# Optimization experiments

Measured on AMD Instinct MI355X. Metric: run time of the kernel, lower is better.

The kernel has to match this reference:

```python
import jax, jax.numpy as jnp
import numpy as np
import math

NH = 12      # num attention heads
WIN = 128    # one-sided sliding window
NG = 32      # number of global (prefix) tokens
NEG = -1e9
LN_EPS = 1e-12


def _layernorm(x, g, b):
    mu = jnp.mean(x, axis=-1, keepdims=True)
    var = jnp.mean(jnp.square(x - mu), axis=-1, keepdims=True)
    return (x - mu) * jax.lax.rsqrt(var + LN_EPS) * g + b


def _longformer_self_attn(h, am, Wq, bq, Wk, bk, Wv, bv):
    B, S, D = h.shape
    Dh = D // NH
    w = WIN
    C = S // w  # number of chunks

    def proj(Wm, bm):
        return (h @ Wm + bm).reshape(B, S, NH, Dh).transpose(0, 2, 1, 3)

    q = proj(Wq, bq) * (1.0 / math.sqrt(Dh))  # [B,H,S,Dh]
    k = proj(Wk, bk)
    v = proj(Wv, bv)

    # ---- banded (sliding window) scores, chunked: each query chunk sees 3w keys ----
    kp = jnp.pad(k, ((0, 0), (0, 0), (w, w), (0, 0)))
    vp = jnp.pad(v, ((0, 0), (0, 0), (w, w), (0, 0)))
    idx = jnp.arange(C)[:, None] * w + jnp.arange(3 * w)[None, :]  # [C,3w]
    k3 = kp[:, :, idx]  # [B,H,C,3w,Dh]
    v3 = vp[:, :, idx]
    qc = q.reshape(B, NH, C, w, Dh)
    band = jnp.einsum('bhcqd,bhckd->bhcqk', qc, k3)  # [B,H,C,w,3w]

    qpos = (jnp.arange(C) * w)[:, None, None] + jnp.arange(w)[None, :, None]  # [C,w,1]
    kpos = (idx - w)[:, None, :]  # [C,1,3w] absolute key positions
    valid = (jnp.abs(kpos - qpos) <= w) & (kpos >= NG) & (kpos < S)  # band, exclude global keys

    amp = jnp.pad(am, ((0, 0), (w, w)))
    am3 = amp[:, idx]  # [B,C,3w] additive mask gathered per chunk
    band = band + am3[:, None, :, None, :]
    band = jnp.where(valid[None, None], band, NEG)
    band = band.reshape(B, NH, S, 3 * w)

    # ---- every token also attends to the NG global tokens ----
    gsc = jnp.einsum('bhsd,bhgd->bhsg', q, k[:, :, :NG]) + am[:, None, None, :NG]

    logits = jnp.concatenate([band, gsc], axis=-1)  # [B,H,S,3w+NG]
    probs = jax.nn.softmax(logits, axis=-1)
    pb = probs[..., :3 * w].reshape(B, NH, C, w, 3 * w)
    out = jnp.einsum('bhcqk,bhckd->bhcqd', pb, v3).reshape(B, NH, S, Dh)
    out = out + jnp.einsum('bhsg,bhgd->bhsd', probs[..., 3 * w:], v[:, :, :NG])

    # ---- global tokens attend to everything ----
    gl = jnp.einsum('bhgd,bhsd->bhgs', q[:, :, :NG], k) + am[:, None, None, :]
    outg = jnp.einsum('bhgs,bhsd->bhgd', jax.nn.softmax(gl, axis=-1), v)

    ctx = jnp.concatenate([outg, out[:, :, NG:]], axis=2)  # [B,H,S,Dh]
    return ctx.transpose(0, 2, 1, 3).reshape(B, S, D)


def setup_inputs() -> dict:
    key = jax.random.key(0)
    ks = jax.random.split(key, 8)
    B, S, D, F = 2, 4096, 768, 3072
    p = lambda k_, sh: jax.random.normal(k_, sh, jnp.float32) * 0.02
    return {
        'hidden_states': jax.random.normal(ks[0], (B, S, D), jnp.float32),
        'attention_mask': jnp.zeros((B, S), jnp.float32),
        'Wq': p(ks[1], (D, D)), 'bq': jnp.zeros((D,), jnp.float32),
        'Wk': p(ks[2], (D, D)), 'bk': jnp.zeros((D,), jnp.float32),
        'Wv': p(ks[3], (D, D)), 'bv': jnp.zeros((D,), jnp.float32),
        'Wo': p(ks[4], (D, D)), 'bo': jnp.zeros((D,), jnp.float32),
        'ln1_g': jnp.ones((D,), jnp.float32), 'ln1_b': jnp.zeros((D,), jnp.float32),
        'Wi': p(ks[5], (D, F)), 'bi': jnp.zeros((F,), jnp.float32),
        'Wo2': p(ks[6], (F, D)), 'bo2': jnp.zeros((D,), jnp.float32),
        'ln2_g': jnp.ones((D,), jnp.float32), 'ln2_b': jnp.zeros((D,), jnp.float32),
    }


def reference(hidden_states, attention_mask, Wq, bq, Wk, bk, Wv, bv, Wo, bo,
              ln1_g, ln1_b, Wi, bi, Wo2, bo2, ln2_g, ln2_b):
    ctx = _longformer_self_attn(hidden_states, attention_mask, Wq, bq, Wk, bk, Wv, bv)
    attn_out = _layernorm(ctx @ Wo + bo + hidden_states, ln1_g, ln1_b)
    inter = jax.nn.gelu(attn_out @ Wi + bi, approximate=False)
    layer_out = _layernorm(inter @ Wo2 + bo2 + attn_out, ln2_g, ln2_b)
    return layer_out
```

## Files before the change

kernel.cpp:

```cpp
#include <hip/hip_runtime.h>
#include <math.h>

#define NHEAD 12
#define DH 64
#define S_LEN 4096
#define B_SZ 2
#define D_MODEL 768
#define FF_DIM 3072
#define WINSZ 128
#define NGLB 32
#define NEGV -1e9f
#define NQC 6291456L

typedef __attribute__((ext_vector_type(8))) short bf16x8;
typedef __attribute__((ext_vector_type(4))) float floatx4;

__device__ __forceinline__ unsigned short f2bf(float x) {
    union { float f; unsigned u; } v; v.f = x;
    unsigned r = v.u + 0x7fffu + ((v.u >> 16) & 1u);
    return (unsigned short)(r >> 16);
}
__device__ __forceinline__ float bf2f(unsigned short x) {
    union { unsigned u; float f; } v; v.u = ((unsigned)x) << 16;
    return v.f;
}

__device__ __forceinline__ void async_copy16(const unsigned short* g, unsigned short* l) {
    __builtin_amdgcn_global_load_lds(
        (const __attribute__((address_space(1))) void*)g,
        (__attribute__((address_space(3))) void*)l, 16, 0, 0);
}

__global__ __launch_bounds__(256) void prep_k(
    const float* __restrict__ Wq, const float* __restrict__ Wk,
    const float* __restrict__ Wv, const float* __restrict__ Wo,
    const float* __restrict__ Wi, const float* __restrict__ Wo2,
    unsigned short* __restrict__ wqt, unsigned short* __restrict__ wkt,
    unsigned short* __restrict__ wvt, unsigned short* __restrict__ wot,
    unsigned short* __restrict__ wit, unsigned short* __restrict__ wo2t,
    const float* __restrict__ bq, const float* __restrict__ bk,
    const float* __restrict__ bv, float* __restrict__ bcat,
    const float* __restrict__ hid, unsigned short* __restrict__ hidb)
{
    __shared__ float tile[32][33];
    const int bid = blockIdx.x;
    const int tx = threadIdx.x, ty = threadIdx.y;

    if (bid < 6912) {
        const float* src; unsigned short* dst; int K, N, nx, local; float scale = 1.f;
        if (bid < 576)       { src = Wq;  dst = wqt;  K = 768;  N = 768;  nx = 24; local = bid;        scale = 0.125f; }
        else if (bid < 1152) { src = Wk;  dst = wkt;  K = 768;  N = 768;  nx = 24; local = bid - 576;  }
        else if (bid < 1728) { src = Wv;  dst = wvt;  K = 768;  N = 768;  nx = 24; local = bid - 1152; }
        else if (bid < 2304) { src = Wo;  dst = wot;  K = 768;  N = 768;  nx = 24; local = bid - 1728; }
        else if (bid < 4608) { src = Wi;  dst = wit;  K = 768;  N = 3072; nx = 96; local = bid - 2304; }
        else                 { src = Wo2; dst = wo2t; K = 3072; N = 768;  nx = 24; local = bid - 4608; }
        const int n0 = (local % nx) * 32, k0 = (local / nx) * 32;
#pragma unroll
        for (int i = 0; i < 4; ++i)
            tile[ty + 8 * i][tx] = src[(long)(k0 + ty + 8 * i) * N + n0 + tx];
        __syncthreads();
#pragma unroll
        for (int i = 0; i < 4; ++i)
            dst[(long)(n0 + ty + 8 * i) * K + k0 + tx] = f2bf(tile[tx][ty + 8 * i] * scale);
    } else if (bid < 6921) {
        const int t = ty * 32 + tx;
        const int i = (bid - 6912) * 256 + t;
        if (i < 768) bcat[i] = bq[i] * 0.125f;
        else if (i < 1536) bcat[i] = bk[i - 768];
        else if (i < 2304) bcat[i] = bv[i - 1536];
    } else {
        const int t = ty * 32 + tx;
        const long i = ((long)(bid - 6921) * 256 + t) * 4;
        float4 v = *(const float4*)(hid + i);
        ushort4 o;
        o.x = f2bf(v.x); o.y = f2bf(v.y); o.z = f2bf(v.z); o.w = f2bf(v.w);
        *(ushort4*)(hidb + i) = o;
    }
}

__global__ __launch_bounds__(256) void vt_k(
    const unsigned short* __restrict__ v, unsigned short* __restrict__ vt)
{
    const int bh = blockIdx.y;
    const int s0 = blockIdx.x * 32;
    const int w = threadIdx.x >> 6, lane = threadIdx.x & 63;
    const unsigned short* src = v + ((long)bh * S_LEN + s0 + w * 8) * DH + lane;
    unsigned short r[8];
#pragma unroll
    for (int j = 0; j < 8; ++j) r[j] = src[j * DH];
    unsigned short* dst = vt + ((long)bh * DH + lane) * S_LEN + s0 + w * 8;
    ushort4 lo, hi;
    lo.x = r[0]; lo.y = r[1]; lo.z = r[2]; lo.w = r[3];
    hi.x = r[4]; hi.y = r[5]; hi.z = r[6]; hi.w = r[7];
    *(ushort4*)dst = lo;
    *(ushort4*)(dst + 4) = hi;
}

template <int EPI>
__global__ __launch_bounds__(256) void gemm_bf(
    const unsigned short* __restrict__ A, const unsigned short* __restrict__ BT,
    const float* __restrict__ bias, void* __restrict__ out,
    int M, int N, int K, int nx)
{
    __shared__ unsigned short As[2][128 * 32];
    __shared__ unsigned short Bs[2][128 * 32];
    const int tid = threadIdx.x;
    const int wave = tid >> 6, lane = tid & 63;
    const int t8 = (blockIdx.x & 7) * (gridDim.x >> 3) + (blockIdx.x >> 3);
    const int m0 = (t8 / nx) * 128, n0 = (t8 % nx) * 128;
    const int wr = (wave >> 1) * 64, wc = (wave & 1) * 64;

    floatx4 acc[4][4];
#pragma unroll
    for (int i = 0; i < 4; ++i)
#pragma unroll
        for (int j = 0; j < 4; ++j) acc[i][j] = (floatx4){0.f, 0.f, 0.f, 0.f};

    const int srow = lane >> 2;
    const int schk = (((lane & 3) ^ (srow & 3))) * 8;
    const int r = lane & 15;
    const int q8 = ((lane >> 4) ^ (lane & 3)) * 8;

    const int NT = K >> 5;
    const unsigned short* aSrc0 = A  + (long)(m0 + wave * 32 + srow) * K + schk;
    const unsigned short* aSrc1 = A  + (long)(m0 + wave * 32 + 16 + srow) * K + schk;
    const unsigned short* bSrc0 = BT + (long)(n0 + wave * 32 + srow) * K + schk;
    const unsigned short* bSrc1 = BT + (long)(n0 + wave * 32 + 16 + srow) * K + schk;
    const int g0 = wave * 1024, g1 = wave * 1024 + 512;

    async_copy16(aSrc0, &As[0][g0]);
    async_copy16(bSrc0, &Bs[0][g0]);
    async_copy16(aSrc1, &As[0][g1]);
    async_copy16(bSrc1, &Bs[0][g1]);
    __syncthreads();

    for (int t = 0; t < NT; ++t) {
        const int cur = t & 1;
        if (t + 1 < NT) {
            const int k0 = (t + 1) << 5;
            async_copy16(aSrc0 + k0, &As[cur ^ 1][g0]);
            async_copy16(bSrc0 + k0, &Bs[cur ^ 1][g0]);
            async_copy16(aSrc1 + k0, &As[cur ^ 1][g1]);
            async_copy16(bSrc1 + k0, &Bs[cur ^ 1][g1]);
        }
        __builtin_amdgcn_sched_barrier(0);

        bf16x8 af[4], bfr[4];
#pragma unroll
        for (int i = 0; i < 4; ++i) {
            af[i]  = *(const bf16x8*)&As[cur][(wr + i * 16 + r) * 32 + q8];
            bfr[i] = *(const bf16x8*)&Bs[cur][(wc + i * 16 + r) * 32 + q8];
        }
        __builtin_amdgcn_s_setprio(1);
#pragma unroll
        for (int i = 0; i < 4; ++i)
#pragma unroll
            for (int j = 0; j < 4; ++j)
                acc[i][j] = __builtin_amdgcn_mfma_f32_16x16x32_bf16(
                    af[i], bfr[j], acc[i][j], 0, 0, 0);
        __builtin_amdgcn_s_setprio(0);
        __syncthreads();
    }

    const int col_l = lane & 15, row_l = (lane >> 4) * 4;
#pragma unroll
    for (int i = 0; i < 4; ++i) {
#pragma unroll
        for (int j = 0; j < 4; ++j) {
            const int n = n0 + wc + j * 16 + col_l;
            const float bv = bias[n];
#pragma unroll
            for (int rg = 0; rg < 4; ++rg) {
                const int m = m0 + wr + i * 16 + row_l + rg;
                float v = acc[i][j][rg] + bv;
                if (EPI == 1) {
                    v = 0.5f * v * (1.f + erff(v * 0.70710678118654752f));
                    ((unsigned short*)out)[(long)m * N + n] = f2bf(v);
                } else {
                    const int bb = m >> 12, s = m & 4095;
                    const int part = n / 768;
                    const int nn = n - part * 768;
                    const int hh = nn >> 6, dh = nn & 63;
                    ((unsigned short*)out)[(long)part * NQC +
                        (((long)bb * NHEAD + hh) * S_LEN + s) * DH + dh] = f2bf(v);
                }
            }
        }
    }
}

__global__ __launch_bounds__(256) void gemm_sp(
    const unsigned short* __restrict__ A, const unsigned short* __restrict__ BT,
    float* __restrict__ p0, float* __restrict__ p1,
    int M, int N, int K2, int nx, int ntile)
{
    __shared__ unsigned short As[2][128 * 32];
    __shared__ unsigned short Bs[2][128 * 32];
    const int tid = threadIdx.x;
    const int wave = tid >> 6, lane = tid & 63;
    const int t8 = (blockIdx.x & 7) * (gridDim.x >> 3) + (blockIdx.x >> 3);
    const int slice = t8 >= ntile;
    const int tile = t8 - slice * ntile;
    const int m0 = (tile / nx) * 128, n0 = (tile % nx) * 128;
    const int kbeg = slice * K2;
    float* P = slice ? p1 : p0;
    const int wr = (wave >> 1) * 64, wc = (wave & 1) * 64;

    floatx4 acc[4][4];
#pragma unroll
    for (int i = 0; i < 4; ++i)
#pragma unroll
        for (int j = 0; j < 4; ++j) acc[i][j] = (floatx4){0.f, 0.f, 0.f, 0.f};

    const int srow = lane >> 2;
    const int schk = (((lane & 3) ^ (srow & 3))) * 8;
    const int r = lane & 15;
    const int q8 = ((lane >> 4) ^ (lane & 3)) * 8;
    const long Kl = (long)K2 * 2;

    const int NT = K2 >> 5;
    const unsigned short* aSrc0 = A  + (long)(m0 + wave * 32 + srow) * Kl + kbeg + schk;
    const unsigned short* aSrc1 = A  + (long)(m0 + wave * 32 + 16 + srow) * Kl + kbeg + schk;
    const unsigned short* bSrc0 = BT + (long)(n0 + wave * 32 + srow) * Kl + kbeg + schk;
    const unsigned short* bSrc1 = BT + (long)(n0 + wave * 32 + 16 + srow) * Kl + kbeg + schk;
    const int g0 = wave * 1024, g1 = wave * 1024 + 512;

    async_copy16(aSrc0, &As[0][g0]);
    async_copy16(bSrc0, &Bs[0][g0]);
    async_copy16(aSrc1, &As[0][g1]);
    async_copy16(bSrc1, &Bs[0][g1]);
    __syncthreads();

    for (int t = 0; t < NT; ++t) {
        const int cur = t & 1;
        if (t + 1 < NT) {
            const int k0 = (t + 1) << 5;
            async_copy16(aSrc0 + k0, &As[cur ^ 1][g0]);
            async_copy16(bSrc0 + k0, &Bs[cur ^ 1][g0]);
            async_copy16(aSrc1 + k0, &As[cur ^ 1][g1]);
            async_copy16(bSrc1 + k0, &Bs[cur ^ 1][g1]);
        }
        __builtin_amdgcn_sched_barrier(0);

        bf16x8 af[4], bfr[4];
#pragma unroll
        for (int i = 0; i < 4; ++i) {
            af[i]  = *(const bf16x8*)&As[cur][(wr + i * 16 + r) * 32 + q8];
            bfr[i] = *(const bf16x8*)&Bs[cur][(wc + i * 16 + r) * 32 + q8];
        }
        __builtin_amdgcn_s_setprio(1);
#pragma unroll
        for (int i = 0; i < 4; ++i)
#pragma unroll
            for (int j = 0; j < 4; ++j)
                acc[i][j] = __builtin_amdgcn_mfma_f32_16x16x32_bf16(
                    af[i], bfr[j], acc[i][j], 0, 0, 0);
        __builtin_amdgcn_s_setprio(0);
        __syncthreads();
    }

    const int col_l = lane & 15, row_l = (lane >> 4) * 4;
#pragma unroll
    for (int i = 0; i < 4; ++i)
#pragma unroll
        for (int j = 0; j < 4; ++j) {
            const int n = n0 + wc + j * 16 + col_l;
#pragma unroll
            for (int rg = 0; rg < 4; ++rg) {
                const int m = m0 + wr + i * 16 + row_l + rg;
                P[(long)m * N + n] = acc[i][j][rg];
            }
        }
}

__global__ __launch_bounds__(256) void attn_k(
    const unsigned short* __restrict__ q, const unsigned short* __restrict__ k,
    const unsigned short* __restrict__ vt, const float* __restrict__ am,
    unsigned short* __restrict__ ctx)
{
    __shared__ __align__(16) unsigned char smem[28800];
    const int blk = blockIdx.x;
    const int tid = threadIdx.x;
    const int wave = tid >> 6, lane = tid & 63;
    const int ln15 = lane & 15, ln4 = lane >> 4;

    if (blk >= 24) {
        unsigned short* Ks = (unsigned short*)smem;
        unsigned short* Vs = Ks + 32 * 72;
        unsigned short* Ps = Vs + 64 * 40;

        const int bb = blk - 24;
        const int c = bb & 31;
        const int h = (bb >> 5) % NHEAD;
        const int b = bb / (32 * NHEAD);
        const long bh = (long)b * NHEAD + h;

        const unsigned short* kh  = k + bh * S_LEN * DH;
        const unsigned short* vth = vt + bh * (long)DH * S_LEN;
        const float* amb = am + (long)b * S_LEN;

        const int q0 = c * WINSZ + wave * 32;

        bf16x8 qf[2][2];
#pragma unroll
        for (int nt = 0; nt < 2; ++nt)
#pragma unroll
            for (int ks = 0; ks < 2; ++ks)
                qf[nt][ks] = *(const bf16x8*)(q + (bh * S_LEN + q0 + nt * 16 + ln15) * DH
                                              + ks * 32 + ln4 * 8);

        floatx4 o[4][2];
#pragma unroll
        for (int mt = 0; mt < 4; ++mt)
#pragma unroll
            for (int nt = 0; nt < 2; ++nt) o[mt][nt] = (floatx4){0.f, 0.f, 0.f, 0.f};
        float m_r[2] = {-1e30f, -1e30f}, l_r[2] = {0.f, 0.f};

        const int sk_key = tid >> 3, sk_ch = tid & 7;
        const int sv_dim = tid & 63, sv_ch = tid >> 6;
        const bf16x8 zero8 = {0, 0, 0, 0, 0, 0, 0, 0};

        for (int tile = 0; tile < 13; ++tile) {
            const bool glob = (tile == 12);
            const int kbase = glob ? 0 : (c * WINSZ - WINSZ + tile * 32);

            __syncthreads();
            {
                int kpos = kbase + sk_key;
                bf16x8 val = zero8;
                if ((unsigned)kpos < (unsigned)S_LEN)
                    val = *(const bf16x8*)(kh + (long)kpos * DH + sk_ch * 8);
                *(bf16x8*)(&Ks[sk_key * 72 + sk_ch * 8]) = val;
            }
            {
                int kc = kbase + sv_ch * 8;
                bf16x8 val = zero8;
                if (kc >= 0 && kc + 8 <= S_LEN)
                    val = *(const bf16x8*)(vth + (long)sv_dim * S_LEN + kc);
                *(bf16x8*)(&Vs[sv_dim * 40 + sv_ch * 8]) = val;
            }
            __syncthreads();

            bf16x8 ak[2][2];
#pragma unroll
            for (int mt = 0; mt < 2; ++mt)
#pragma unroll
                for (int ks = 0; ks < 2; ++ks)
                    ak[mt][ks] = *(const bf16x8*)(&Ks[(mt * 16 + ln15) * 72 + ks * 32 + ln4 * 8]);

            floatx4 s[2][2];
#pragma unroll
            for (int mt = 0; mt < 2; ++mt)
#pragma unroll
                for (int nt = 0; nt < 2; ++nt) {
                    floatx4 acc = (floatx4){0.f, 0.f, 0.f, 0.f};
                    acc = __builtin_amdgcn_mfma_f32_16x16x32_bf16(ak[mt][0], qf[nt][0], acc, 0, 0, 0);
                    acc = __builtin_amdgcn_mfma_f32_16x16x32_bf16(ak[mt][1], qf[nt][1], acc, 0, 0, 0);
                    s[mt][nt] = acc;
                }

#pragma unroll
            for (int mt = 0; mt < 2; ++mt) {
                const int kp0 = kbase + mt * 16 + ln4 * 4;
#pragma unroll
                for (int rg = 0; rg < 4; ++rg) {
                    const int kpos = kp0 + rg;
                    const bool kin = (unsigned)kpos < (unsigned)S_LEN;
                    const float amv = kin ? amb[kpos] : 0.f;
#pragma unroll
                    for (int nt = 0; nt < 2; ++nt) {
                        const int qpos = q0 + nt * 16 + ln15;
                        const int dlt = kpos > qpos ? kpos - qpos : qpos - kpos;
                        const bool valid = glob || (kpos >= NGLB && kin && dlt <= WINSZ);
                        s[mt][nt][rg] = valid ? s[mt][nt][rg] + amv : NEGV;
                    }
                }
            }

            float alpha[2];
#pragma unroll
            for (int nt = 0; nt < 2; ++nt) {
                float mx = s[0][nt][0];
#pragma unroll
                for (int rg = 1; rg < 4; ++rg) mx = fmaxf(mx, s[0][nt][rg]);
#pragma unroll
                for (int rg = 0; rg < 4; ++rg) mx = fmaxf(mx, s[1][nt][rg]);
                mx = fmaxf(mx, __shfl_xor(mx, 16));
                mx = fmaxf(mx, __shfl_xor(mx, 32));
                const float mn = fmaxf(m_r[nt], mx);
                alpha[nt] = __expf(m_r[nt] - mn);
                m_r[nt] = mn;
            }

#pragma unroll
            for (int nt = 0; nt < 2; ++nt) {
                float sum = 0.f;
#pragma unroll
                for (int mt = 0; mt < 2; ++mt) {
                    ushort4 pk;
#pragma unroll
                    for (int rg = 0; rg < 4; ++rg) {
                        const float p = __expf(s[mt][nt][rg] - m_r[nt]);
                        sum += p;
                        ((unsigned short*)&pk)[rg] = f2bf(p);
                    }
                    *(ushort4*)(&Ps[wave * 1280 + (nt * 16 + ln15) * 40 + mt * 16 + ln4 * 4]) = pk;
                }
                sum += __shfl_xor(sum, 16);
                sum += __shfl_xor(sum, 32);
                l_r[nt] = l_r[nt] * alpha[nt] + sum;
            }

#pragma unroll
            for (int mt = 0; mt < 4; ++mt)
#pragma unroll
                for (int nt = 0; nt < 2; ++nt)
#pragma unroll
                    for (int rg = 0; rg < 4; ++rg) o[mt][nt][rg] *= alpha[nt];

            bf16x8 av[4], bp[2];
#pragma unroll
            for (int mt = 0; mt < 4; ++mt)
                av[mt] = *(const bf16x8*)(&Vs[(mt * 16 + ln15) * 40 + ln4 * 8]);
#pragma unroll
            for (int nt = 0; nt < 2; ++nt)
                bp[nt] = *(const bf16x8*)(&Ps[wave * 1280 + (nt * 16 + ln15) * 40 + ln4 * 8]);
#pragma unroll
            for (int mt = 0; mt < 4; ++mt)
#pragma unroll
                for (int nt = 0; nt < 2; ++nt)
                    o[mt][nt] = __builtin_amdgcn_mfma_f32_16x16x32_bf16(
                        av[mt], bp[nt], o[mt][nt], 0, 0, 0);
        }

        if (q0 >= NGLB) {
            const float inv0 = 1.f / l_r[0], inv1 = 1.f / l_r[1];
#pragma unroll
            for (int nt = 0; nt < 2; ++nt) {
                const float inv = nt ? inv1 : inv0;
                const long row = (long)b * S_LEN + q0 + nt * 16 + ln15;
#pragma unroll
                for (int mt = 0; mt < 4; ++mt) {
                    ushort4 ov;
#pragma unroll
                    for (int rg = 0; rg < 4; ++rg)
                        ((unsigned short*)&ov)[rg] = f2bf(o[mt][nt][rg] * inv);
                    *(ushort4*)(ctx + row * D_MODEL + h * DH + mt * 16 + ln4 * 4) = ov;
                }
            }
        }
    } else {
        unsigned short* Psg = (unsigned short*)smem;
        float* Om   = (float*)(smem + 18432);
        float* mW   = (float*)(smem + 27648);
        float* lW   = (float*)(smem + 28160);
        float* lTot = (float*)(smem + 28672);

        const int bh = blk;
        const int b = bh / NHEAD, h = bh % NHEAD;

        const unsigned short* kh  = k + (long)bh * S_LEN * DH;
        const unsigned short* vth = vt + (long)bh * DH * S_LEN;
        const float* amb = am + (long)b * S_LEN;

        bf16x8 qf[2][2];
#pragma unroll
        for (int nt = 0; nt < 2; ++nt)
#pragma unroll
            for (int ks = 0; ks < 2; ++ks)
                qf[nt][ks] = *(const bf16x8*)(q + ((long)bh * S_LEN + nt * 16 + ln15) * DH
                                              + ks * 32 + ln4 * 8);

        floatx4 o[4][2];
#pragma unroll
        for (int mt = 0; mt < 4; ++mt)
#pragma unroll
            for (int nt = 0; nt < 2; ++nt) o[mt][nt] = (floatx4){0.f, 0.f, 0.f, 0.f};
        float m_r[2] = {-1e30f, -1e30f}, l_r[2] = {0.f, 0.f};

        for (int it = 0; it < 16; ++it) {
            const int kbase = it * 256 + wave * 64;

            bf16x8 ak[4][2];
#pragma unroll
            for (int mt = 0; mt < 4; ++mt)
#pragma unroll
                for (int ks = 0; ks < 2; ++ks)
                    ak[mt][ks] = *(const bf16x8*)(kh + (long)(kbase + mt * 16 + ln15) * DH
                                                  + ks * 32 + ln4 * 8);

            floatx4 s[4][2];
#pragma unroll
            for (int mt = 0; mt < 4; ++mt)
#pragma unroll
                for (int nt = 0; nt < 2; ++nt) {
                    floatx4 acc = (floatx4){0.f, 0.f, 0.f, 0.f};
                    acc = __builtin_amdgcn_mfma_f32_16x16x32_bf16(ak[mt][0], qf[nt][0], acc, 0, 0, 0);
                    acc = __builtin_amdgcn_mfma_f32_16x16x32_bf16(ak[mt][1], qf[nt][1], acc, 0, 0, 0);
                    s[mt][nt] = acc;
                }

#pragma unroll
            for (int mt = 0; mt < 4; ++mt) {
                const int kp0 = kbase + mt * 16 + ln4 * 4;
#pragma unroll
                for (int rg = 0; rg < 4; ++rg) {
                    const float amv = amb[kp0 + rg];
#pragma unroll
                    for (int nt = 0; nt < 2; ++nt) s[mt][nt][rg] += amv;
                }
            }

            float alpha[2];
#pragma unroll
            for (int nt = 0; nt < 2; ++nt) {
                float mx = s[0][nt][0];
#pragma unroll
                for (int mt = 0; mt < 4; ++mt)
#pragma unroll
                    for (int rg = 0; rg < 4; ++rg) mx = fmaxf(mx, s[mt][nt][rg]);
                mx = fmaxf(mx, __shfl_xor(mx, 16));
                mx = fmaxf(mx, __shfl_xor(mx, 32));
                const float mn = fmaxf(m_r[nt], mx);
                alpha[nt] = __expf(m_r[nt] - mn);
                m_r[nt] = mn;
            }

#pragma unroll
            for (int nt = 0; nt < 2; ++nt) {
                float sum = 0.f;
#pragma unroll
                for (int mt = 0; mt < 4; ++mt) {
                    ushort4 pk;
#pragma unroll
                    for (int rg = 0; rg < 4; ++rg) {
                        const float p = __expf(s[mt][nt][rg] - m_r[nt]);
                        sum += p;
                        ((unsigned short*)&pk)[rg] = f2bf(p);
                    }
                    *(ushort4*)(&Psg[wave * 2304 + (nt * 16 + ln15) * 72 + mt * 16 + ln4 * 4]) = pk;
                }
                sum += __shfl_xor(sum, 16);
                sum += __shfl_xor(sum, 32);
                l_r[nt] = l_r[nt] * alpha[nt] + sum;
            }

#pragma unroll
            for (int mt = 0; mt < 4; ++mt)
#pragma unroll
                for (int nt = 0; nt < 2; ++nt)
#pragma unroll
                    for (int rg = 0; rg < 4; ++rg) o[mt][nt][rg] *= alpha[nt];

            bf16x8 av[4][2], bp[2][2];
#pragma unroll
            for (int mt = 0; mt < 4; ++mt)
#pragma unroll
                for (int ks = 0; ks < 2; ++ks)
                    av[mt][ks] = *(const bf16x8*)(vth + (long)(mt * 16 + ln15) * S_LEN
                                                  + kbase + ks * 32 + ln4 * 8);
#pragma unroll
            for (int nt = 0; nt < 2; ++nt)
#pragma unroll
                for (int ks = 0; ks < 2; ++ks)
                    bp[nt][ks] = *(const bf16x8*)(&Psg[wave * 2304 + (nt * 16 + ln15) * 72
                                                  + ks * 32 + ln4 * 8]);
#pragma unroll
            for (int mt = 0; mt < 4; ++mt)
#pragma unroll
                for (int nt = 0; nt < 2; ++nt) {
                    o[mt][nt] = __builtin_amdgcn_mfma_f32_16x16x32_bf16(
                        av[mt][0], bp[nt][0], o[mt][nt], 0, 0, 0);
                    o[mt][nt] = __builtin_amdgcn_mfma_f32_16x16x32_bf16(
                        av[mt][1], bp[nt][1], o[mt][nt], 0, 0, 0);
                }
        }

        if (ln4 == 0) {
#pragma unroll
            for (int nt = 0; nt < 2; ++nt) {
                mW[wave * 32 + nt * 16 + ln15] = m_r[nt];
                lW[wave * 32 + nt * 16 + ln15] = l_r[nt];
            }
        }
        for (int i = tid; i < 64 * 36; i += 256) Om[i] = 0.f;
        __syncthreads();

        float f[2];
#pragma unroll
        for (int nt = 0; nt < 2; ++nt) {
            const int qq = nt * 16 + ln15;
            float mt_ = mW[qq];
#pragma unroll
            for (int w = 1; w < 4; ++w) mt_ = fmaxf(mt_, mW[w * 32 + qq]);
            float lt = 0.f;
#pragma unroll
            for (int w = 0; w < 4; ++w) lt += __expf(mW[w * 32 + qq] - mt_) * lW[w * 32 + qq];
            f[nt] = __expf(m_r[nt] - mt_);
            if (wave == 0 && ln4 == 0) lTot[qq] = lt;
        }
#pragma unroll
        for (int mt = 0; mt < 4; ++mt)
#pragma unroll
            for (int nt = 0; nt < 2; ++nt)
#pragma unroll
                for (int rg = 0; rg < 4; ++rg) o[mt][nt][rg] *= f[nt];

        for (int wv = 0; wv < 4; ++wv) {
            if (wave == wv) {
#pragma unroll
                for (int mt = 0; mt < 4; ++mt)
#pragma unroll
                    for (int nt = 0; nt < 2; ++nt)
#pragma unroll
                        for (int rg = 0; rg < 4; ++rg)
                            Om[(mt * 16 + ln4 * 4 + rg) * 36 + nt * 16 + ln15] += o[mt][nt][rg];
            }
            __syncthreads();
        }

        const int qq = tid >> 3, d0 = (tid & 7) * 8;
        const float inv = 1.f / lTot[qq];
        ushort4 ov0, ov1;
#pragma unroll
        for (int i = 0; i < 4; ++i)
            ((unsigned short*)&ov0)[i] = f2bf(Om[(d0 + i) * 36 + qq] * inv);
#pragma unroll
        for (int i = 0; i < 4; ++i)
            ((unsigned short*)&ov1)[i] = f2bf(Om[(d0 + 4 + i) * 36 + qq] * inv);
        unsigned short* dst = ctx + ((long)b * S_LEN + qq) * D_MODEL + h * DH + d0;
        *(ushort4*)dst = ov0;
        *(ushort4*)(dst + 4) = ov1;
    }
}

__global__ __launch_bounds__(256) void ln2p_k(
    const float* __restrict__ p0, const float* __restrict__ p1,
    const float* __restrict__ bias, const float* __restrict__ resid,
    float* __restrict__ out, unsigned short* __restrict__ out_bf,
    const float* __restrict__ gw, const float* __restrict__ bw)
{
    __shared__ float red[8];
    const long base = (long)blockIdx.x * D_MODEL;
    const int t = threadIdx.x;
    const int wv = t >> 6, lane = t & 63;
    float v0 = p0[base + t]       + p1[base + t]       + bias[t]       + resid[base + t];
    float v1 = p0[base + t + 256] + p1[base + t + 256] + bias[t + 256] + resid[base + t + 256];
    float v2 = p0[base + t + 512] + p1[base + t + 512] + bias[t + 512] + resid[base + t + 512];

    float s = v0 + v1 + v2;
#pragma unroll
    for (int off = 32; off; off >>= 1) s += __shfl_xor(s, off);
    if (lane == 0) red[wv] = s;
    __syncthreads();
    const float mu = (red[0] + red[1] + red[2] + red[3]) * (1.f / 768.f);

    const float d0 = v0 - mu, d1 = v1 - mu, d2 = v2 - mu;
    float s2 = d0 * d0 + d1 * d1 + d2 * d2;
#pragma unroll
    for (int off = 32; off; off >>= 1) s2 += __shfl_xor(s2, off);
    if (lane == 0) red[4 + wv] = s2;
    __syncthreads();
    const float var = (red[4] + red[5] + red[6] + red[7]) * (1.f / 768.f);
    const float rs = rsqrtf(var + 1e-12f);

    const float y0 = d0 * rs * gw[t] + bw[t];
    const float y1 = d1 * rs * gw[t + 256] + bw[t + 256];
    const float y2 = d2 * rs * gw[t + 512] + bw[t + 512];
    if (out) {
        float* y = out + base;
        y[t] = y0; y[t + 256] = y1; y[t + 512] = y2;
    }
    if (out_bf) {
        unsigned short* yb = out_bf + base;
        yb[t] = f2bf(y0); yb[t + 256] = f2bf(y1); yb[t + 512] = f2bf(y2);
    }
}

extern "C" void kernel_launch(void* const* d_in, const int* in_sizes, int n_in,
                              void* d_out, int out_size, void* d_ws, size_t ws_size,
                              hipStream_t stream)
{
    const float* hid  = (const float*)d_in[0];
    const float* am   = (const float*)d_in[1];
    const float* Wq   = (const float*)d_in[2];
    const float* bq   = (const float*)d_in[3];
    const float* Wk   = (const float*)d_in[4];
    const float* bk   = (const float*)d_in[5];
    const float* Wv   = (const float*)d_in[6];
    const float* bv   = (const float*)d_in[7];
    const float* Wo   = (const float*)d_in[8];
    const float* bo   = (const float*)d_in[9];
    const float* ln1g = (const float*)d_in[10];
    const float* ln1b = (const float*)d_in[11];
    const float* Wi   = (const float*)d_in[12];
    const float* bi   = (const float*)d_in[13];
    const float* Wo2  = (const float*)d_in[14];
    const float* bo2  = (const float*)d_in[15];
    const float* ln2g = (const float*)d_in[16];
    const float* ln2b = (const float*)d_in[17];

    const long M  = (long)B_SZ * S_LEN;
    const long NQ = NQC;

    unsigned short* W16 = (unsigned short*)d_ws;
    unsigned short* qb   = W16;
    unsigned short* kb   = W16 + NQ;
    unsigned short* vb   = W16 + 2 * NQ;
    unsigned short* vtb  = W16 + 3 * NQ;
    unsigned short* ctxb = W16 + 4 * NQ;
    unsigned short* hidb = W16 + 5 * NQ;
    unsigned short* wqt  = W16 + 6 * NQ;
    unsigned short* wkt  = wqt + 589824;
    unsigned short* wvt  = wkt + 589824;
    unsigned short* wot  = wvt + 589824;
    unsigned short* wit  = wot + 589824;
    unsigned short* wo2t = wit + 2359296;
    float* tmp   = (float*)(W16 + 44826624);
    float* partB1 = (float*)(W16 + 57409536);
    float* bcat  = (float*)(W16 + 69992448);
    float* partA0 = (float*)W16;
    float* partA1 = (float*)(W16 + 2 * NQ);
    unsigned short* interb = W16;
    unsigned short* attnb  = hidb;
    float* partB0 = (float*)(W16 + 4 * NQ);
    (void)ws_size; (void)in_sizes; (void)n_in; (void)out_size;

    prep_k<<<dim3(13065), dim3(32, 8), 0, stream>>>(
        Wq, Wk, Wv, Wo, Wi, Wo2, wqt, wkt, wvt, wot, wit, wo2t,
        bq, bk, bv, bcat, hid, hidb);

    dim3 blk(256);

    gemm_bf<2><<<dim3(1152), blk, 0, stream>>>(hidb, wqt, bcat, qb,
                                               M, 2304, 768, 18);

    vt_k<<<dim3(128, 24), blk, 0, stream>>>(vb, vtb);

    attn_k<<<dim3(792), blk, 0, stream>>>(qb, kb, vtb, am, ctxb);

    gemm_sp<<<dim3(768), blk, 0, stream>>>(ctxb, wot, partA0, partA1,
                                           M, 768, 384, 6, 384);
    ln2p_k<<<dim3(M), blk, 0, stream>>>(partA0, partA1, bo, hid,
                                        tmp, attnb, ln1g, ln1b);

    gemm_bf<1><<<dim3(1536), blk, 0, stream>>>(attnb, wit, bi, interb,
                                               M, 3072, 768, 24);

    gemm_sp<<<dim3(768), blk, 0, stream>>>(interb, wo2t, partB0, partB1,
                                           M, 768, 1536, 6, 384);
    ln2p_k<<<dim3(M), blk, 0, stream>>>(partB0, partB1, bo2, tmp,
                                        (float*)d_out, nullptr, ln2g, ln2b);
}
```

Measured before the change: 411.9 us.

## Triple-buffer GEMM shared-memory tiles with partial vmcnt waits

```diff
diff --git a/kernel.cpp b/kernel.cpp
--- a/kernel.cpp
+++ b/kernel.cpp
@@ -102,8 +102,8 @@
     const float* __restrict__ bias, void* __restrict__ out,
     int M, int N, int K, int nx)
 {
-    __shared__ unsigned short As[2][128 * 32];
-    __shared__ unsigned short Bs[2][128 * 32];
+    __shared__ unsigned short As[3][128 * 32];
+    __shared__ unsigned short Bs[3][128 * 32];
     const int tid = threadIdx.x;
     const int wave = tid >> 6, lane = tid & 63;
     const int t8 = (blockIdx.x & 7) * (gridDim.x >> 3) + (blockIdx.x >> 3);
@@ -132,16 +132,27 @@
     async_copy16(bSrc0, &Bs[0][g0]);
     async_copy16(aSrc1, &As[0][g1]);
     async_copy16(bSrc1, &Bs[0][g1]);
-    __syncthreads();
-
+    if (NT > 1) {
+        async_copy16(aSrc0 + 32, &As[1][g0]);
+        async_copy16(bSrc0 + 32, &Bs[1][g0]);
+        async_copy16(aSrc1 + 32, &As[1][g1]);
+        async_copy16(bSrc1 + 32, &Bs[1][g1]);
+        asm volatile("s_waitcnt vmcnt(4)" ::: "memory");
+    } else {
+        asm volatile("s_waitcnt vmcnt(0)" ::: "memory");
+    }
+    __builtin_amdgcn_s_barrier();
+    __builtin_amdgcn_sched_barrier(0);
+
+    int cur = 0;
     for (int t = 0; t < NT; ++t) {
-        const int cur = t & 1;
-        if (t + 1 < NT) {
-            const int k0 = (t + 1) << 5;
-            async_copy16(aSrc0 + k0, &As[cur ^ 1][g0]);
-            async_copy16(bSrc0 + k0, &Bs[cur ^ 1][g0]);
-            async_copy16(aSrc1 + k0, &As[cur ^ 1][g1]);
-            async_copy16(bSrc1 + k0, &Bs[cur ^ 1][g1]);
+        if (t + 2 < NT) {
+            int nb = cur + 2; if (nb >= 3) nb -= 3;
+            const int k0 = (t + 2) << 5;
+            async_copy16(aSrc0 + k0, &As[nb][g0]);
+            async_copy16(bSrc0 + k0, &Bs[nb][g0]);
+            async_copy16(aSrc1 + k0, &As[nb][g1]);
+            async_copy16(bSrc1 + k0, &Bs[nb][g1]);
         }
         __builtin_amdgcn_sched_barrier(0);
 
@@ -159,7 +170,16 @@
                 acc[i][j] = __builtin_amdgcn_mfma_f32_16x16x32_bf16(
                     af[i], bfr[j], acc[i][j], 0, 0, 0);
         __builtin_amdgcn_s_setprio(0);
-        __syncthreads();
+        __builtin_amdgcn_sched_barrier(0);
+        if (t + 2 < NT) {
+            asm volatile("s_waitcnt vmcnt(4)" ::: "memory");
+            __builtin_amdgcn_s_barrier();
+        } else if (t + 1 < NT) {
+            asm volatile("s_waitcnt vmcnt(0)" ::: "memory");
+            __builtin_amdgcn_s_barrier();
+        }
+        __builtin_amdgcn_sched_barrier(0);
+        if (++cur == 3) cur = 0;
     }
 
     const int col_l = lane & 15, row_l = (lane >> 4) * 4;
@@ -194,8 +214,8 @@
     float* __restrict__ p0, float* __restrict__ p1,
     int M, int N, int K2, int nx, int ntile)
 {
-    __shared__ unsigned short As[2][128 * 32];
-    __shared__ unsigned short Bs[2][128 * 32];
+    __shared__ unsigned short As[3][128 * 32];
+    __shared__ unsigned short Bs[3][128 * 32];
     const int tid = threadIdx.x;
     const int wave = tid >> 6, lane = tid & 63;
     const int t8 = (blockIdx.x & 7) * (gridDim.x >> 3) + (blockIdx.x >> 3);
@@ -229,16 +249,27 @@
     async_copy16(bSrc0, &Bs[0][g0]);
     async_copy16(aSrc1, &As[0][g1]);
     async_copy16(bSrc1, &Bs[0][g1]);
-    __syncthreads();
-
+    if (NT > 1) {
+        async_copy16(aSrc0 + 32, &As[1][g0]);
+        async_copy16(bSrc0 + 32, &Bs[1][g0]);
+        async_copy16(aSrc1 + 32, &As[1][g1]);
+        async_copy16(bSrc1 + 32, &Bs[1][g1]);
+        asm volatile("s_waitcnt vmcnt(4)" ::: "memory");
+    } else {
+        asm volatile("s_waitcnt vmcnt(0)" ::: "memory");
+    }
+    __builtin_amdgcn_s_barrier();
+    __builtin_amdgcn_sched_barrier(0);
+
+    int cur = 0;
     for (int t = 0; t < NT; ++t) {
-        const int cur = t & 1;
-        if (t + 1 < NT) {
-            const int k0 = (t + 1) << 5;
-            async_copy16(aSrc0 + k0, &As[cur ^ 1][g0]);
-            async_copy16(bSrc0 + k0, &Bs[cur ^ 1][g0]);
-            async_copy16(aSrc1 + k0, &As[cur ^ 1][g1]);
-            async_copy16(bSrc1 + k0, &Bs[cur ^ 1][g1]);
+        if (t + 2 < NT) {
+            int nb = cur + 2; if (nb >= 3) nb -= 3;
+            const int k0 = (t + 2) << 5;
+            async_copy16(aSrc0 + k0, &As[nb][g0]);
+            async_copy16(bSrc0 + k0, &Bs[nb][g0]);
+            async_copy16(aSrc1 + k0, &As[nb][g1]);
+            async_copy16(bSrc1 + k0, &Bs[nb][g1]);
         }
         __builtin_amdgcn_sched_barrier(0);
 
@@ -256,7 +287,16 @@
                 acc[i][j] = __builtin_amdgcn_mfma_f32_16x16x32_bf16(
                     af[i], bfr[j], acc[i][j], 0, 0, 0);
         __builtin_amdgcn_s_setprio(0);
-        __syncthreads();
+        __builtin_amdgcn_sched_barrier(0);
+        if (t + 2 < NT) {
+            asm volatile("s_waitcnt vmcnt(4)" ::: "memory");
+            __builtin_amdgcn_s_barrier();
+        } else if (t + 1 < NT) {
+            asm volatile("s_waitcnt vmcnt(0)" ::: "memory");
+            __builtin_amdgcn_s_barrier();
+        }
+        __builtin_amdgcn_sched_barrier(0);
+        if (++cur == 3) cur = 0;
     }
 
     const int col_l = lane & 15, row_l = (lane >> 4) * 4;
```

New measurement: 410.1 us. No clear change (-0.4%).

## Triple-buffer GEMM LDS staging with partial vmcnt waits and unrolled-by-3 loop

Applied to the files above, without the earlier changes.

```diff
diff --git a/kernel.cpp b/kernel.cpp
--- a/kernel.cpp
+++ b/kernel.cpp
@@ -96,14 +96,48 @@
     *(ushort4*)(dst + 4) = hi;
 }
 
+#define GEMM_BODY(U, PF, TAILW)                                              \
+    {                                                                        \
+        if (PF) {                                                            \
+            async_copy16(aSrc0 + (U + 2) * 32, &As[(U + 2) % 3][g0]);        \
+            async_copy16(bSrc0 + (U + 2) * 32, &Bs[(U + 2) % 3][g0]);        \
+            async_copy16(aSrc1 + (U + 2) * 32, &As[(U + 2) % 3][g1]);        \
+            async_copy16(bSrc1 + (U + 2) * 32, &Bs[(U + 2) % 3][g1]);        \
+        }                                                                    \
+        __builtin_amdgcn_sched_barrier(0);                                   \
+        bf16x8 af[4], bfr[4];                                                \
+        _Pragma("unroll")                                                    \
+        for (int i = 0; i < 4; ++i) {                                        \
+            af[i]  = *(const bf16x8*)&As[U][rdA + i * 512];                  \
+            bfr[i] = *(const bf16x8*)&Bs[U][rdB + i * 512];                  \
+        }                                                                    \
+        __builtin_amdgcn_s_setprio(1);                                       \
+        _Pragma("unroll")                                                    \
+        for (int i = 0; i < 4; ++i)                                          \
+            _Pragma("unroll")                                                \
+            for (int j = 0; j < 4; ++j)                                      \
+                acc[i][j] = __builtin_amdgcn_mfma_f32_16x16x32_bf16(         \
+                    af[i], bfr[j], acc[i][j], 0, 0, 0);                      \
+        __builtin_amdgcn_s_setprio(0);                                       \
+        __builtin_amdgcn_sched_barrier(0);                                   \
+        if (TAILW == 2) {                                                    \
+            asm volatile("s_waitcnt vmcnt(4)" ::: "memory");                 \
+            __builtin_amdgcn_s_barrier();                                    \
+        } else if (TAILW == 1) {                                             \
+            asm volatile("s_waitcnt vmcnt(0)" ::: "memory");                 \
+            __builtin_amdgcn_s_barrier();                                    \
+        }                                                                    \
+        __builtin_amdgcn_sched_barrier(0);                                   \
+    }
+
 template <int EPI>
 __global__ __launch_bounds__(256) void gemm_bf(
     const unsigned short* __restrict__ A, const unsigned short* __restrict__ BT,
     const float* __restrict__ bias, void* __restrict__ out,
     int M, int N, int K, int nx)
 {
-    __shared__ unsigned short As[2][128 * 32];
-    __shared__ unsigned short Bs[2][128 * 32];
+    __shared__ unsigned short As[3][128 * 32];
+    __shared__ unsigned short Bs[3][128 * 32];
     const int tid = threadIdx.x;
     const int wave = tid >> 6, lane = tid & 63;
     const int t8 = (blockIdx.x & 7) * (gridDim.x >> 3) + (blockIdx.x >> 3);
@@ -120,6 +154,8 @@
     const int schk = (((lane & 3) ^ (srow & 3))) * 8;
     const int r = lane & 15;
     const int q8 = ((lane >> 4) ^ (lane & 3)) * 8;
+    const int rdA = (wr + r) * 32 + q8;
+    const int rdB = (wc + r) * 32 + q8;
 
     const int NT = K >> 5;
     const unsigned short* aSrc0 = A  + (long)(m0 + wave * 32 + srow) * K + schk;
@@ -132,35 +168,23 @@
     async_copy16(bSrc0, &Bs[0][g0]);
     async_copy16(aSrc1, &As[0][g1]);
     async_copy16(bSrc1, &Bs[0][g1]);
-    __syncthreads();
-
-    for (int t = 0; t < NT; ++t) {
-        const int cur = t & 1;
-        if (t + 1 < NT) {
-            const int k0 = (t + 1) << 5;
-            async_copy16(aSrc0 + k0, &As[cur ^ 1][g0]);
-            async_copy16(bSrc0 + k0, &Bs[cur ^ 1][g0]);
-            async_copy16(aSrc1 + k0, &As[cur ^ 1][g1]);
-            async_copy16(bSrc1 + k0, &Bs[cur ^ 1][g1]);
-        }
-        __builtin_amdgcn_sched_barrier(0);
-
-        bf16x8 af[4], bfr[4];
-#pragma unroll
-        for (int i = 0; i < 4; ++i) {
-            af[i]  = *(const bf16x8*)&As[cur][(wr + i * 16 + r) * 32 + q8];
-            bfr[i] = *(const bf16x8*)&Bs[cur][(wc + i * 16 + r) * 32 + q8];
-        }
-        __builtin_amdgcn_s_setprio(1);
-#pragma unroll
-        for (int i = 0; i < 4; ++i)
-#pragma unroll
-            for (int j = 0; j < 4; ++j)
-                acc[i][j] = __builtin_amdgcn_mfma_f32_16x16x32_bf16(
-                    af[i], bfr[j], acc[i][j], 0, 0, 0);
-        __builtin_amdgcn_s_setprio(0);
-        __syncthreads();
+    async_copy16(aSrc0 + 32, &As[1][g0]);
+    async_copy16(bSrc0 + 32, &Bs[1][g0]);
+    async_copy16(aSrc1 + 32, &As[1][g1]);
+    async_copy16(bSrc1 + 32, &Bs[1][g1]);
+    asm volatile("s_waitcnt vmcnt(4)" ::: "memory");
+    __builtin_amdgcn_s_barrier();
+    __builtin_amdgcn_sched_barrier(0);
+
+    for (int t3 = 0; t3 < NT - 3; t3 += 3) {
+        GEMM_BODY(0, 1, 2)
+        GEMM_BODY(1, 1, 2)
+        GEMM_BODY(2, 1, 2)
+        aSrc0 += 96; aSrc1 += 96; bSrc0 += 96; bSrc1 += 96;
     }
+    GEMM_BODY(0, 1, 2)
+    GEMM_BODY(1, 0, 1)
+    GEMM_BODY(2, 0, 0)
 
     const int col_l = lane & 15, row_l = (lane >> 4) * 4;
 #pragma unroll
@@ -194,8 +218,8 @@
     float* __restrict__ p0, float* __restrict__ p1,
     int M, int N, int K2, int nx, int ntile)
 {
-    __shared__ unsigned short As[2][128 * 32];
-    __shared__ unsigned short Bs[2][128 * 32];
+    __shared__ unsigned short As[3][128 * 32];
+    __shared__ unsigned short Bs[3][128 * 32];
     const int tid = threadIdx.x;
     const int wave = tid >> 6, lane = tid & 63;
     const int t8 = (blockIdx.x & 7) * (gridDim.x >> 3) + (blockIdx.x >> 3);
@@ -216,6 +240,8 @@
     const int schk = (((lane & 3) ^ (srow & 3))) * 8;
     const int r = lane & 15;
     const int q8 = ((lane >> 4) ^ (lane & 3)) * 8;
+    const int rdA = (wr + r) * 32 + q8;
+    const int rdB = (wc + r) * 32 + q8;
     const long Kl = (long)K2 * 2;
 
     const int NT = K2 >> 5;
@@ -229,35 +255,23 @@
     async_copy16(bSrc0, &Bs[0][g0]);
     async_copy16(aSrc1, &As[0][g1]);
     async_copy16(bSrc1, &Bs[0][g1]);
-    __syncthreads();
-
-    for (int t = 0; t < NT; ++t) {
-        const int cur = t & 1;
-        if (t + 1 < NT) {
-            const int k0 = (t + 1) << 5;
-            async_copy16(aSrc0 + k0, &As[cur ^ 1][g0]);
-            async_copy16(bSrc0 + k0, &Bs[cur ^ 1][g0]);
-            async_copy16(aSrc1 + k0, &As[cur ^ 1][g1]);
-            async_copy16(bSrc1 + k0, &Bs[cur ^ 1][g1]);
-        }
-        __builtin_amdgcn_sched_barrier(0);
-
-        bf16x8 af[4], bfr[4];
-#pragma unroll
-        for (int i = 0; i < 4; ++i) {
-            af[i]  = *(const bf16x8*)&As[cur][(wr + i * 16 + r) * 32 + q8];
-            bfr[i] = *(const bf16x8*)&Bs[cur][(wc + i * 16 + r) * 32 + q8];
-        }
-        __builtin_amdgcn_s_setprio(1);
-#pragma unroll
-        for (int i = 0; i < 4; ++i)
-#pragma unroll
-            for (int j = 0; j < 4; ++j)
-                acc[i][j] = __builtin_amdgcn_mfma_f32_16x16x32_bf16(
-                    af[i], bfr[j], acc[i][j], 0, 0, 0);
-        __builtin_amdgcn_s_setprio(0);
-        __syncthreads();
+    async_copy16(aSrc0 + 32, &As[1][g0]);
+    async_copy16(bSrc0 + 32, &Bs[1][g0]);
+    async_copy16(aSrc1 + 32, &As[1][g1]);
+    async_copy16(bSrc1 + 32, &Bs[1][g1]);
+    asm volatile("s_waitcnt vmcnt(4)" ::: "memory");
+    __builtin_amdgcn_s_barrier();
+    __builtin_amdgcn_sched_barrier(0);
+
+    for (int t3 = 0; t3 < NT - 3; t3 += 3) {
+        GEMM_BODY(0, 1, 2)
+        GEMM_BODY(1, 1, 2)
+        GEMM_BODY(2, 1, 2)
+        aSrc0 += 96; aSrc1 += 96; bSrc0 += 96; bSrc1 += 96;
     }
+    GEMM_BODY(0, 1, 2)
+    GEMM_BODY(1, 0, 1)
+    GEMM_BODY(2, 0, 0)
 
     const int col_l = lane & 15, row_l = (lane >> 4) * 4;
 #pragma unroll
```

Result: no change. 405.2 us (-1.6%).
